# Optimization experiments

Measured on AMD Instinct MI355X. Metric: run time of the kernel, lower is better.

Reference implementation:

```python
import jax, jax.numpy as jnp
import numpy as np

FILL = -1000.0


def setup_inputs() -> dict:
    key = jax.random.key(0)
    k1, k2, k3 = jax.random.split(key, 3)
    B, T, L = 512, 512, 126
    emissions = jax.random.normal(k1, (B, T, L), dtype=jnp.float32)
    labels = jax.random.randint(k2, (B, T), 0, L, dtype=jnp.int32)
    transitions = jax.random.normal(k3, (L + 2, L + 2), dtype=jnp.float32)
    # mask: nothing transitions INTO start; nothing transitions OUT of end
    transitions = transitions.at[:, L].set(FILL).at[L + 1, :].set(FILL)
    return {"emissions": emissions, "labels": labels, "transitions": transitions}


def _expand_emission(emission, L):
    # emission: [T, L] -> [T+2, L+2] with START/END pseudo-observations
    T = emission.shape[0]
    pad = jnp.full((T, 2), FILL, dtype=emission.dtype)
    e = jnp.concatenate([emission, pad], axis=1)
    b_s = jnp.full((1, L + 2), FILL, dtype=emission.dtype).at[0, L].set(0.0)
    e_s = jnp.full((1, L + 2), FILL, dtype=emission.dtype).at[0, L + 1].set(0.0)
    return jnp.concatenate([b_s, e, e_s], axis=0)


def _total_path_score(emission, transitions, L):
    # Faithful to the original _log_sum_exp: per-column max, but the log term
    # sums exp over the WHOLE matrix (scalar), added to every column max.
    E = _expand_emission(emission, L)  # [T+2, L+2]

    def step(pre, obs):
        score = obs[None, :] + pre[:, None] + transitions  # [L+2, L+2]
        m = jnp.max(score, axis=0)                         # [L+2]
        pre_new = m + jnp.log(jnp.sum(jnp.exp(score - m[None, :])))
        return pre_new, None

    pre, _ = jax.lax.scan(step, E[0], E[1:])
    m = jnp.max(pre)
    return m + jnp.log(jnp.sum(jnp.exp(pre - m)))


def _real_path_score(emission, labels, transitions, L):
    T = emission.shape[0]
    em = jnp.sum(emission[jnp.arange(T), labels])
    seq = jnp.concatenate([
        jnp.array([L], dtype=labels.dtype), labels,
        jnp.array([L + 1], dtype=labels.dtype)
    ])
    tr = jnp.sum(transitions[seq[:-1], seq[1:]])
    return em + tr


def reference(emissions, labels, transitions):
    L = emissions.shape[-1]
    total = jax.vmap(lambda e: _total_path_score(e, transitions, L))(emissions)
    real = jax.vmap(lambda e, y: _real_path_score(e, y, transitions, L))(emissions, labels)
    return jnp.sum(total - real)
```

## Files before the change

### kernel.cpp

```cpp
#include <hip/hip_runtime.h>
#include <hip/hip_fp16.h>

#define NB 512
#define NT 512
#define NL 126
#define NS 128
#define SIGMA 0.0625f

typedef _Float16 h2 __attribute__((ext_vector_type(2)));

static __device__ __forceinline__ int pk_from(float a, float b) {
  return __builtin_bit_cast(int, __builtin_amdgcn_cvt_pkrtz(a, b));
}
static __device__ __forceinline__ int pkmul(int a, int b) {
  int d; asm("v_pk_mul_f16 %0, %1, %2" : "=v"(d) : "v"(a), "v"(b)); return d;
}
static __device__ __forceinline__ int pkmax(int a, int b) {
  int d; asm("v_pk_max_f16 %0, %1, %2" : "=v"(d) : "v"(a), "v"(b)); return d;
}
static __device__ __forceinline__ int pkadd(int a, int b) {
  int d; asm("v_pk_add_f16 %0, %1, %2" : "=v"(d) : "v"(a), "v"(b)); return d;
}
static __device__ __forceinline__ int dppswap(int x) {
  return __builtin_amdgcn_update_dpp(0, x, 0xB1, 0xf, 0xf, false);
}

#define DPP_ADD(x, ctrl, rm) \
  ((x) + __int_as_float(__builtin_amdgcn_update_dpp(0, __float_as_int(x), (ctrl), (rm), 0xf, false)))
#define WAVE_ADD(x) do { \
  x = DPP_ADD(x, 0x111, 0xf); x = DPP_ADD(x, 0x112, 0xf); \
  x = DPP_ADD(x, 0x114, 0xf); x = DPP_ADD(x, 0x118, 0xf); \
  x = DPP_ADD(x, 0x142, 0xa); x = DPP_ADD(x, 0x143, 0xc); } while (0)

__global__ __launch_bounds__(256) void crf_kernel(
    const float* __restrict__ emissions,
    const int*   __restrict__ labels,
    const float* __restrict__ trans,
    float*       __restrict__ out)
{
  const int b   = blockIdx.x;
  const int tid = threadIdx.x;
  const int wv  = tid >> 6;
  const int ln  = tid & 63;
  const int col = (wv << 5) | (ln >> 1);
  const int rh  = ln & 1;

  __shared__ __align__(16) _Float16 u_sh[2 * NS];
  __shared__ __align__(16) float sPart[2][4];
  __shared__ __align__(16) float zPart[2][4];
  __shared__ float fin[4];

  const float* em  = emissions + (size_t)b * NT * NL;
  const int*   lab = labels + b * NT;

  float tau = -3.0e38f;
  for (int i = 0; i < NS; i++) tau = fmaxf(tau, trans[i * NS + col]);

  int tab[32];
  #pragma unroll
  for (int k = 0; k < 32; k++) {
    int row = rh * 64 + 2 * k;
    float t0 = __expf(trans[row * NS + col] - tau);
    float t1 = __expf(trans[(row + 1) * NS + col] - tau);
    tab[k] = pk_from(t0, t1);
  }

  float realp = 0.f;
  #pragma unroll
  for (int q = 0; q < NT / 256; q++) {
    int t  = tid + q * 256;
    int lt = lab[t];
    int nx = (t + 1 < NT) ? lab[t + 1] : (NL + 1);
    realp += em[t * NL + lt] + trans[lt * NS + nx];
  }
  if (tid == 0) realp += trans[NL * NS + lab[0]];

  if (tid < NS) {
    u_sh[tid]      = (_Float16)((tid == NL) ? 1.f : 0.f);
    u_sh[NS + tid] = (_Float16)0.f;
  }
  float Q = 0.f, Cc = 0.f;
  float emc = (col < NL) ? em[col] : 0.f;
  float emn = (col < NL) ? em[NL + col] : 0.f;
  __syncthreads();

  for (int t = 0; t <= NT; t++) {
    float r;
    if (t > 0) {
      const float4 sp = *(const float4*)sPart[t & 1];
      const float4 zp = *(const float4*)zPart[t & 1];
      float S = 0.5f * ((sp.x + sp.y) + (sp.z + sp.w));
      float Z = 0.5f * ((zp.x + zp.y) + (zp.z + zp.w));
      Cc += __logf(S);
      Q  += __logf(Z);
      r = SIGMA * __builtin_amdgcn_rcpf(Z);
    } else {
      r = SIGMA;
    }

    float obsv;
    if (t < NT) obsv = (col < NL) ? emc : -1000.f;
    else        obsv = (col == NL + 1) ? 0.f : -1000.f;
    float g = __expf(obsv + tau);
    float emf = (t + 2 < NT && col < NL) ? em[(t + 2) * NL + col] : 0.f;
    emc = emn; emn = emf;

    const int4* up = (const int4*)(u_sh + (t & 1) * NS) + rh * 8;
    int hA = 0, hB = 0, hC = 0, hD = 0;
    int sA = 0, sB = 0, sC = 0, sD = 0;
    #pragma unroll
    for (int kk = 0; kk < 8; kk++) {
      int4 uu = up[kk];
      int m0 = pkmul(uu.x, tab[4 * kk + 0]);
      int m1 = pkmul(uu.y, tab[4 * kk + 1]);
      int m2 = pkmul(uu.z, tab[4 * kk + 2]);
      int m3 = pkmul(uu.w, tab[4 * kk + 3]);
      hA = pkmax(hA, m0); hB = pkmax(hB, m1);
      hC = pkmax(hC, m2); hD = pkmax(hD, m3);
      sA = pkadd(sA, m0); sB = pkadd(sB, m1);
      sC = pkadd(sC, m2); sD = pkadd(sD, m3);
    }
    int hv = pkmax(pkmax(hA, hB), pkmax(hC, hD));
    int sv = pkadd(pkadd(sA, sB), pkadd(sC, sD));
    hv = pkmax(hv, dppswap(hv));
    sv = pkadd(sv, dppswap(sv));
    h2 hh = __builtin_bit_cast(h2, hv);
    h2 ss = __builtin_bit_cast(h2, sv);
    float h = fmaxf(fmaxf((float)hh.x, (float)hh.y), 1e-30f);
    float s = (float)ss.x + (float)ss.y;

    float w = h * g;
    float v = w * r;
    u_sh[((t + 1) & 1) * NS + col] = (_Float16)v;

    float contrib = s * __builtin_amdgcn_rcpf(h);
    float cS = contrib, cV = v;
    WAVE_ADD(cS);
    WAVE_ADD(cV);
    if (ln == 63) {
      sPart[(t + 1) & 1][wv] = cS;
      zPart[(t + 1) & 1][wv] = cV;
    }
    __syncthreads();
  }

  {
    const float4 sp = *(const float4*)sPart[1];
    const float4 zp = *(const float4*)zPart[1];
    float S = 0.5f * ((sp.x + sp.y) + (sp.z + sp.w));
    float Z = 0.5f * ((zp.x + zp.y) + (zp.z + zp.w));
    Cc += __logf(S);
    Q  += __logf(Z);
  }

  WAVE_ADD(realp);
  if (ln == 63) fin[wv] = realp;
  __syncthreads();
  if (tid == 0) {
    const float CONST = 513.f * 2.772588722f;
    float total = Cc + Q + CONST;
    atomicAdd(out, total - ((fin[0] + fin[1]) + (fin[2] + fin[3])));
  }
}

extern "C" void kernel_launch(void* const* d_in, const int* in_sizes, int n_in,
                              void* d_out, int out_size, void* d_ws, size_t ws_size,
                              hipStream_t stream) {
  const float* em  = (const float*)d_in[0];
  const int*   lab = (const int*)d_in[1];
  const float* tr  = (const float*)d_in[2];
  (void)hipMemsetAsync(d_out, 0, sizeof(float), stream);
  crf_kernel<<<NB, 256, 0, stream>>>(em, lab, tr, (float*)d_out);
}
```

Measured before the change: 634.4 us.

## Compute normalizer locally from shared vector and defer S reduction off critical path

Each thread now computes the normalizer Z itself by summing the shared u vector in fp16 packed adds, instead of reducing it through a cross-wave DPP reduction and shared-memory partials. The S-contribution wave reduction is deferred by one step, so it overlaps with the next iteration rather than sitting before the barrier. Together these remove one wave reduction from each step's critical path. SIGMA is lowered to keep the fp16 magnitudes in range, which trades some extra precision risk in the fp16 Z sums and changes how the final log terms are assembled.

```diff
diff --git a/kernel.cpp b/kernel.cpp
--- a/kernel.cpp
+++ b/kernel.cpp
@@ -5,7 +5,8 @@
 #define NT 512
 #define NL 126
 #define NS 128
-#define SIGMA 0.0625f
+#define SIGMA 0.015625f
+#define LOG_INV_SIGMA 4.158883083f
 
 typedef _Float16 h2 __attribute__((ext_vector_type(2)));
 
@@ -47,8 +48,7 @@
 
   __shared__ __align__(16) _Float16 u_sh[2 * NS];
   __shared__ __align__(16) float sPart[2][4];
-  __shared__ __align__(16) float zPart[2][4];
-  __shared__ float fin[4];
+  __shared__ float fin[8];
 
   const float* em  = emissions + (size_t)b * NT * NL;
   const int*   lab = labels + b * NT;
@@ -82,35 +82,37 @@
   float Q = 0.f, Cc = 0.f;
   float emc = (col < NL) ? em[col] : 0.f;
   float emn = (col < NL) ? em[NL + col] : 0.f;
+  float cSprev = 0.f, vlast = 0.f;
   __syncthreads();
 
   for (int t = 0; t <= NT; t++) {
-    float r;
     if (t > 0) {
+      float cs = cSprev;
+      WAVE_ADD(cs);
+      if (ln == 63) sPart[(t - 1) & 1][wv] = cs;
+    }
+    if (t >= 2) {
       const float4 sp = *(const float4*)sPart[t & 1];
-      const float4 zp = *(const float4*)zPart[t & 1];
       float S = 0.5f * ((sp.x + sp.y) + (sp.z + sp.w));
-      float Z = 0.5f * ((zp.x + zp.y) + (zp.z + zp.w));
       Cc += __logf(S);
-      Q  += __logf(Z);
-      r = SIGMA * __builtin_amdgcn_rcpf(Z);
-    } else {
-      r = SIGMA;
     }
 
     float obsv;
     if (t < NT) obsv = (col < NL) ? emc : -1000.f;
     else        obsv = (col == NL + 1) ? 0.f : -1000.f;
     float g = __expf(obsv + tau);
-    float emf = (t + 2 < NT && col < NL) ? em[(t + 2) * NL + col] : 0.f;
-    emc = emn; emn = emf;
+    emc = emn;
+    emn = (t + 2 < NT && col < NL) ? em[(t + 2) * NL + col] : 0.f;
 
     const int4* up = (const int4*)(u_sh + (t & 1) * NS) + rh * 8;
     int hA = 0, hB = 0, hC = 0, hD = 0;
     int sA = 0, sB = 0, sC = 0, sD = 0;
+    int zA = 0, zB = 0;
     #pragma unroll
     for (int kk = 0; kk < 8; kk++) {
       int4 uu = up[kk];
+      zA = pkadd(zA, pkadd(uu.x, uu.y));
+      zB = pkadd(zB, pkadd(uu.z, uu.w));
       int m0 = pkmul(uu.x, tab[4 * kk + 0]);
       int m1 = pkmul(uu.y, tab[4 * kk + 1]);
       int m2 = pkmul(uu.z, tab[4 * kk + 2]);
@@ -122,44 +124,52 @@
     }
     int hv = pkmax(pkmax(hA, hB), pkmax(hC, hD));
     int sv = pkadd(pkadd(sA, sB), pkadd(sC, sD));
+    int zv = pkadd(zA, zB);
     hv = pkmax(hv, dppswap(hv));
     sv = pkadd(sv, dppswap(sv));
+    zv = pkadd(zv, dppswap(zv));
     h2 hh = __builtin_bit_cast(h2, hv);
     h2 ss = __builtin_bit_cast(h2, sv);
+    h2 zh = __builtin_bit_cast(h2, zv);
     float h = fmaxf(fmaxf((float)hh.x, (float)hh.y), 1e-30f);
     float s = (float)ss.x + (float)ss.y;
+    float Z = fmaxf((float)zh.x + (float)zh.y, 1e-30f);
+
+    float r = SIGMA * __builtin_amdgcn_rcpf(Z);
+    Q += __logf(Z);
 
     float w = h * g;
     float v = w * r;
+    vlast = v;
     u_sh[((t + 1) & 1) * NS + col] = (_Float16)v;
 
-    float contrib = s * __builtin_amdgcn_rcpf(h);
-    float cS = contrib, cV = v;
-    WAVE_ADD(cS);
-    WAVE_ADD(cV);
-    if (ln == 63) {
-      sPart[(t + 1) & 1][wv] = cS;
-      zPart[(t + 1) & 1][wv] = cV;
-    }
+    cSprev = s * __builtin_amdgcn_rcpf(h);
     __syncthreads();
   }
 
   {
-    const float4 sp = *(const float4*)sPart[1];
-    const float4 zp = *(const float4*)zPart[1];
+    float cs = cSprev;
+    WAVE_ADD(cs);
+    if (ln == 63) sPart[NT & 1][wv] = cs;
+    const float4 sp = *(const float4*)sPart[(NT - 1) & 1];
     float S = 0.5f * ((sp.x + sp.y) + (sp.z + sp.w));
-    float Z = 0.5f * ((zp.x + zp.y) + (zp.z + zp.w));
     Cc += __logf(S);
-    Q  += __logf(Z);
   }
-
-  WAVE_ADD(realp);
-  if (ln == 63) fin[wv] = realp;
+  {
+    float vf = vlast;
+    WAVE_ADD(vf);
+    WAVE_ADD(realp);
+    if (ln == 63) { fin[wv] = vf; fin[4 + wv] = realp; }
+  }
   __syncthreads();
   if (tid == 0) {
-    const float CONST = 513.f * 2.772588722f;
-    float total = Cc + Q + CONST;
-    atomicAdd(out, total - ((fin[0] + fin[1]) + (fin[2] + fin[3])));
+    const float4 sp = *(const float4*)sPart[NT & 1];
+    float S = 0.5f * ((sp.x + sp.y) + (sp.z + sp.w));
+    float Cfin = Cc + __logf(S);
+    float Zf = 0.5f * ((fin[0] + fin[1]) + (fin[2] + fin[3]));
+    float realsum = (fin[4] + fin[5]) + (fin[6] + fin[7]);
+    float total = Cfin + Q + 513.f * LOG_INV_SIGMA + __logf(Zf);
+    atomicAdd(out, total - realsum);
   }
 }
 
```

Result: slower. 706.1 us (+11.3%).
